# Kernel tuning notes

Hardware: AMD Instinct MI355X
Metric: run time of the kernel (lower is better)

Reference implementation:

```python
import jax, jax.numpy as jnp
import numpy as np

B, C, H, W = 2, 512, 64, 64
NUM_GROUPS = 32
EPS = 1e-6


def setup_inputs() -> dict:
    key = jax.random.key(0)
    ks = jax.random.split(key, 6)
    s = 1.0 / np.sqrt(C)
    return {
        "x": jax.random.normal(ks[0], (B, C, H, W), dtype=jnp.float32),
        "gn_scale": jnp.ones((C,), jnp.float32),
        "gn_bias": jnp.zeros((C,), jnp.float32),
        "wq": jax.random.normal(ks[1], (C, C), jnp.float32) * s,
        "bq": jnp.zeros((C,), jnp.float32),
        "wk": jax.random.normal(ks[2], (C, C), jnp.float32) * s,
        "bk": jnp.zeros((C,), jnp.float32),
        "wv": jax.random.normal(ks[3], (C, C), jnp.float32) * s,
        "bv": jnp.zeros((C,), jnp.float32),
        "wp": jax.random.normal(ks[4], (C, C), jnp.float32) * s,
        "bp": jnp.zeros((C,), jnp.float32),
    }


def group_norm(x, scale, bias):
    # x: [b, c, h, w]; GroupNorm with NUM_GROUPS groups, eps=1e-6, affine
    b, c, h, w = x.shape
    xg = x.reshape(b, NUM_GROUPS, c // NUM_GROUPS, h, w)
    mean = jnp.mean(xg, axis=(2, 3, 4), keepdims=True)
    var = jnp.var(xg, axis=(2, 3, 4), keepdims=True)
    xg = (xg - mean) * jax.lax.rsqrt(var + EPS)
    xn = xg.reshape(b, c, h, w)
    return xn * scale[None, :, None, None] + bias[None, :, None, None]


def reference(x, gn_scale, gn_bias, wq, bq, wk, bk, wv, bv, wp, bp):
    b, c, h, w = x.shape
    n = h * w
    hn = group_norm(x, gn_scale, gn_bias).reshape(b, c, n)  # [b,c,n]
    # 1x1 convs == per-pixel linear over channels
    q = jnp.einsum('dc,bcn->bdn', wq, hn) + bq[None, :, None]
    k = jnp.einsum('dc,bcn->bdn', wk, hn) + bk[None, :, None]
    v = jnp.einsum('dc,bcn->bdn', wv, hn) + bv[None, :, None]
    # attn[b,i,j] = softmax_j( q[:, :, i] . k[:, :, j] / sqrt(c) )
    attn = jnp.einsum('bci,bcj->bij', q, k) * (float(c) ** -0.5)
    attn = jax.nn.softmax(attn, axis=-1)
    out = jnp.einsum('bcj,bij->bci', v, attn)  # [b,c,n]
    out = jnp.einsum('dc,bcn->bdn', wp, out) + bp[None, :, None]
    return x + out.reshape(b, c, h, w)
```

## Files before the change

kernel.cpp:

```cpp
#include <hip/hip_runtime.h>

typedef __bf16 bf16x8 __attribute__((ext_vector_type(8)));
typedef float f32x4 __attribute__((ext_vector_type(4)));
typedef int i32x8 __attribute__((ext_vector_type(8)));


#if defined(__has_builtin)
#if __has_builtin(__builtin_amdgcn_global_load_lds)
#define HAS_GLL 1
#endif
#endif

__device__ __forceinline__ void async_copy16(const void* g, void* l) {
#ifdef HAS_GLL
    __builtin_amdgcn_global_load_lds(
        (const __attribute__((address_space(1))) unsigned int*)g,
        (__attribute__((address_space(3))) unsigned int*)l, 16, 0, 0);
#else
    *(int4*)l = *(const int4*)g;
#endif
}

__device__ __forceinline__ unsigned char to_fp8(float v) {
    return (unsigned char)(__builtin_amdgcn_cvt_pk_fp8_f32(v, v, 0, false) & 0xFF);
}

#define MXSCALE 0x7F7F7F7F

__global__ __launch_bounds__(256) void prep_kernel(
    const float* __restrict__ x, float* __restrict__ ps,
    const float* __restrict__ wq, const float* __restrict__ wk,
    const float* __restrict__ wv, const float* __restrict__ wp,
    const float* __restrict__ bq, const float* __restrict__ bk,
    unsigned char* __restrict__ wqk8, unsigned char* __restrict__ wv8,
    __bf16* __restrict__ wp_b, float* __restrict__ bqk) {
    if (blockIdx.x >= 1024) {
        int idx = (blockIdx.x - 1024) * 256 + threadIdx.x;
        wqk8[idx] = to_fp8(wq[idx]);
        wqk8[262144 + idx] = to_fp8(wk[idx]);
        wv8[idx] = to_fp8(wv[idx]);
        wp_b[idx] = (__bf16)wp[idx];
        if (idx < 512) {
            bqk[idx] = bq[idx];
            bqk[512 + idx] = bk[idx];
        }
        return;
    }
    int blk = blockIdx.x;
    const float4* base = (const float4*)x + (size_t)blk * 1024;
    float s1 = 0.f, s2 = 0.f;
#pragma unroll
    for (int i = 0; i < 4; ++i) {
        float4 v = base[threadIdx.x + (i << 8)];
        s1 += v.x + v.y + v.z + v.w;
        s2 += v.x * v.x + v.y * v.y + v.z * v.z + v.w * v.w;
    }
    for (int off = 32; off >= 1; off >>= 1) {
        s1 += __shfl_xor(s1, off);
        s2 += __shfl_xor(s2, off);
    }
    __shared__ float r1[4], r2[4];
    int wave = threadIdx.x >> 6, lane = threadIdx.x & 63;
    if (lane == 0) { r1[wave] = s1; r2[wave] = s2; }
    __syncthreads();
    if (threadIdx.x == 0) {
        ps[blk] = r1[0] + r1[1] + r1[2] + r1[3];
        ps[1024 + blk] = r2[0] + r2[1] + r2[2] + r2[3];
    }
}

__global__ __launch_bounds__(256) void gn_apply_kernel(const float* __restrict__ x,
                                                       const float* __restrict__ gn_scale,
                                                       const float* __restrict__ gn_bias,
                                                       const float* __restrict__ ps,
                                                       unsigned char* __restrict__ hn8) {
    __shared__ float tile[32][33];
    int b = blockIdx.z;
    int n0 = blockIdx.x * 32, c0 = blockIdx.y * 32;
    int tx = threadIdx.x & 31, ty = threadIdx.x >> 5;
    const float* xb = x + (size_t)b * 512 * 4096;
#pragma unroll
    for (int r = 0; r < 4; ++r) {
        int c = ty + r * 8;
        tile[c][tx] = xb[(size_t)(c0 + c) * 4096 + n0 + tx];
    }
    int c = c0 + tx;
    int g = (b << 5) + (c >> 4);
    float s1 = 0.f, s2 = 0.f;
#pragma unroll
    for (int i = 0; i < 16; ++i) {
        s1 += ps[(g << 4) + i];
        s2 += ps[1024 + (g << 4) + i];
    }
    float m = s1 * (1.f / 65536.f);
    float var = s2 * (1.f / 65536.f) - m * m;
    float rs = rsqrtf(var + 1e-6f);
    float sc = gn_scale[c] * rs;
    float bi = gn_bias[c] - m * sc;
    __syncthreads();
    unsigned char* outp = hn8 + (size_t)b * 4096 * 512;
#pragma unroll
    for (int r = 0; r < 4; ++r) {
        int n = ty + r * 8;
        float v = tile[tx][n];
        outp[(size_t)(n0 + n) * 512 + c] = to_fp8(v * sc + bi);
    }
}

template <int BN, int OUT_MODE, int BIAS_MODE>
__device__ __forceinline__ void mx_gemm_body(
    const unsigned char* __restrict__ Ab, int lda,
    const unsigned char* __restrict__ Bb, int ldb,
    void* __restrict__ C, int ldc,
    const float* __restrict__ bias, int K, float scale,
    long m0, long n0, unsigned char* As, unsigned char* Bs) {
    constexpr int NT = BN / 32;
    constexpr int BSZ = BN * 128;
    const int tid = threadIdx.x;
    const int lane = tid & 63, wave = tid >> 6;
    const int ln = lane & 15, q = lane >> 4;
    const int wm = (wave >> 1) << 6;
    const int wn = (wave & 1) * (BN / 2);

    f32x4 acc[4][NT] = {};

#pragma unroll
    for (int p = 0; p < 4; ++p) {
        int c = (p << 8) + tid;
        int row = c >> 3, sg = ((c & 7) ^ (row & 7)) << 4;
        async_copy16(Ab + (long)row * lda + sg, &As[c << 4]);
    }
#pragma unroll
    for (int p = 0; p < NT; ++p) {
        int c = (p << 8) + tid;
        int row = c >> 3, sg = ((c & 7) ^ (row & 7)) << 4;
        async_copy16(Bb + (long)row * ldb + sg, &Bs[c << 4]);
    }

    const int nk = K >> 7;
    for (int ki = 0; ki < nk; ++ki) {
        __syncthreads();
        const int cur = ki & 1;
        if (ki + 1 < nk) {
            const int k1 = (ki + 1) << 7;
            unsigned char* Ad = As + (cur ^ 1) * 16384;
            unsigned char* Bd = Bs + (cur ^ 1) * BSZ;
#pragma unroll
            for (int p = 0; p < 4; ++p) {
                int c = (p << 8) + tid;
                int row = c >> 3, sg = ((c & 7) ^ (row & 7)) << 4;
                async_copy16(Ab + (long)row * lda + k1 + sg, Ad + (c << 4));
            }
#pragma unroll
            for (int p = 0; p < NT; ++p) {
                int c = (p << 8) + tid;
                int row = c >> 3, sg = ((c & 7) ^ (row & 7)) << 4;
                async_copy16(Bb + (long)row * ldb + k1 + sg, Bd + (c << 4));
            }
        }
        const unsigned char* Ar = As + cur * 16384;
        const unsigned char* Br = Bs + cur * BSZ;
        i32x8 af[4], bf[NT];
#pragma unroll
        for (int t = 0; t < 4; ++t) {
            int row = wm + t * 16 + ln, e = row & 7;
            const unsigned char* ap = Ar + (row << 7);
            *(int4*)&af[t] = *(const int4*)(ap + ((((q << 1)) ^ e) << 4));
            *((int4*)&af[t] + 1) = *(const int4*)(ap + ((((q << 1) | 1) ^ e) << 4));
        }
#pragma unroll
        for (int t = 0; t < NT; ++t) {
            int row = wn + t * 16 + ln, e = row & 7;
            const unsigned char* bp = Br + (row << 7);
            *(int4*)&bf[t] = *(const int4*)(bp + ((((q << 1)) ^ e) << 4));
            *((int4*)&bf[t] + 1) = *(const int4*)(bp + ((((q << 1) | 1) ^ e) << 4));
        }
#pragma unroll
        for (int mt = 0; mt < 4; ++mt)
#pragma unroll
            for (int nt = 0; nt < NT; ++nt)
                acc[mt][nt] = __builtin_amdgcn_mfma_scale_f32_16x16x128_f8f6f4(
                    af[mt], bf[nt], acc[mt][nt], 0, 0, 0, MXSCALE, 0, MXSCALE);
    }

#pragma unroll
    for (int mt = 0; mt < 4; ++mt) {
#pragma unroll
        for (int nt = 0; nt < NT; ++nt) {
            long col = n0 + wn + nt * 16 + ln;
#pragma unroll
            for (int r = 0; r < 4; ++r) {
                long row = m0 + wm + mt * 16 + (q << 2) + r;
                float v = acc[mt][nt][r] * scale;
                if (BIAS_MODE == 1) v += bias[row];
                if (BIAS_MODE == 2) v += bias[col];
                long off = row * (long)ldc + col;
                if (OUT_MODE == 0) {
                    ((unsigned char*)C)[off] = to_fp8(v);
                } else {
                    ((_Float16*)C)[off] = (_Float16)v;
                }
            }
        }
    }
}

__global__ __launch_bounds__(256) void qkv_kernel(
    const unsigned char* __restrict__ hn8, const unsigned char* __restrict__ wqk8,
    const unsigned char* __restrict__ wv8, const float* __restrict__ bqk,
    const float* __restrict__ bv, unsigned char* __restrict__ qk8,
    unsigned char* __restrict__ v8) {
    __shared__ __align__(16) unsigned char As[2 * 128 * 128];
    __shared__ __align__(16) unsigned char Bs[2 * 128 * 128];
    int z = blockIdx.z;
    if (z < 2) {
        long b = z;
        long m0 = (long)blockIdx.y * 128, n0 = (long)blockIdx.x * 128;
        mx_gemm_body<128, 0, 2>(hn8 + b * 4096 * 512 + m0 * 512, 512,
                                wqk8 + n0 * 512, 512,
                                qk8 + b * 4096 * 1024, 1024,
                                bqk, 512, 1.f, m0, n0, As, Bs);
    } else {
        long b = z - 2;
        int flat = blockIdx.y * 8 + blockIdx.x;
        long m0 = (long)(flat >> 6) * 128, n0 = (long)(flat & 63) * 64;
        mx_gemm_body<64, 0, 1>(wv8 + m0 * 512, 512,
                               hn8 + b * 4096 * 512 + n0 * 512, 512,
                               v8 + b * 512 * 4096, 4096,
                               bv, 512, 1.f, m0, n0, As, Bs);
    }
}

__global__ __launch_bounds__(256) void mx_s_kernel(const unsigned char* __restrict__ QK,
                                                   unsigned char* __restrict__ S,
                                                   float scale) {
    __shared__ __align__(16) unsigned char As[2 * 128 * 128];
    __shared__ __align__(16) unsigned char Bs[2 * 128 * 128];
    long b = blockIdx.z;
    long m0 = (long)blockIdx.y * 128, n0 = (long)blockIdx.x * 128;
    mx_gemm_body<128, 0, 0>(QK + b * 4096 * 1024 + m0 * 1024, 1024,
                            QK + b * 4096 * 1024 + n0 * 1024 + 512, 1024,
                            S + b * 4096 * 4096, 4096,
                            nullptr, 512, scale, m0, n0, As, Bs);
}

#define CVT4(dst, base, word)                                   \
    dst[base + 0] = __builtin_amdgcn_cvt_f32_fp8(word, 0);      \
    dst[base + 1] = __builtin_amdgcn_cvt_f32_fp8(word, 1);      \
    dst[base + 2] = __builtin_amdgcn_cvt_f32_fp8(word, 2);      \
    dst[base + 3] = __builtin_amdgcn_cvt_f32_fp8(word, 3);

__global__ __launch_bounds__(256) void softmax_kernel(unsigned char* __restrict__ S) {
    long row = blockIdx.x;
    unsigned char* srow = S + (row << 12);
    int tid = threadIdx.x;
    int4 d = ((const int4*)srow)[tid];
    float v[16];
    CVT4(v, 0, d.x)
    CVT4(v, 4, d.y)
    CVT4(v, 8, d.z)
    CVT4(v, 12, d.w)
    float mx = -1e30f;
#pragma unroll
    for (int p = 0; p < 16; ++p) mx = fmaxf(mx, v[p]);
    for (int off = 32; off >= 1; off >>= 1) mx = fmaxf(mx, __shfl_xor(mx, off));
    __shared__ float red[4], red2[4];
    int wave = tid >> 6, lane = tid & 63;
    if (lane == 0) red[wave] = mx;
    __syncthreads();
    mx = fmaxf(fmaxf(red[0], red[1]), fmaxf(red[2], red[3]));
    float s = 0.f;
#pragma unroll
    for (int p = 0; p < 16; ++p) {
        v[p] = __expf(v[p] - mx);
        s += v[p];
    }
    for (int off = 32; off >= 1; off >>= 1) s += __shfl_xor(s, off);
    if (lane == 0) red2[wave] = s;
    __syncthreads();
    s = red2[0] + red2[1] + red2[2] + red2[3];
    float inv64 = 64.f / s;
    int w[4];
#pragma unroll
    for (int i = 0; i < 4; ++i) {
        w[i] = __builtin_amdgcn_cvt_pk_fp8_f32(v[4 * i] * inv64, v[4 * i + 1] * inv64, 0, false);
        w[i] = __builtin_amdgcn_cvt_pk_fp8_f32(v[4 * i + 2] * inv64, v[4 * i + 3] * inv64, w[i], true);
    }
    ((int4*)srow)[tid] = make_int4(w[0], w[1], w[2], w[3]);
}

__global__ __launch_bounds__(256) void mx_pv_kernel(const unsigned char* __restrict__ P,
                                                    const unsigned char* __restrict__ V,
                                                    __bf16* __restrict__ O) {
    __shared__ __align__(16) unsigned char As[2 * 128 * 128];
    __shared__ __align__(16) unsigned char Bs[2 * 64 * 128];
    const int tid = threadIdx.x;
    const int lane = tid & 63, wave = tid >> 6;
    const int ln = lane & 15, q = lane >> 4;
    const int wm = (wave >> 1) << 6, wn = (wave & 1) << 5;
    const int b = blockIdx.x >> 5;
    const long m0 = (long)(blockIdx.x & 31) * 128;
    const long n0 = (long)blockIdx.y * 64;
    const unsigned char* Pb = P + ((long)b * 4096 + m0) * 4096;
    const unsigned char* Vb = V + ((long)b * 512 + n0) * 4096;

    f32x4 acc[4][2] = {};

#pragma unroll
    for (int p = 0; p < 4; ++p) {
        int c = (p << 8) + tid;
        int row = c >> 3, sg = ((c & 7) ^ (row & 7)) << 4;
        async_copy16(Pb + (long)row * 4096 + sg, &As[c << 4]);
    }
#pragma unroll
    for (int p = 0; p < 2; ++p) {
        int c = (p << 8) + tid;
        int row = c >> 3, sg = ((c & 7) ^ (row & 7)) << 4;
        async_copy16(Vb + (long)row * 4096 + sg, &Bs[c << 4]);
    }

    for (int ki = 0; ki < 32; ++ki) {
        __syncthreads();
        const int cur = ki & 1;
        if (ki + 1 < 32) {
            const int k1 = (ki + 1) << 7;
            unsigned char* Ad = As + (cur ^ 1) * 16384;
            unsigned char* Bd = Bs + (cur ^ 1) * 8192;
#pragma unroll
            for (int p = 0; p < 4; ++p) {
                int c = (p << 8) + tid;
                int row = c >> 3, sg = ((c & 7) ^ (row & 7)) << 4;
                async_copy16(Pb + (long)row * 4096 + k1 + sg, Ad + (c << 4));
            }
#pragma unroll
            for (int p = 0; p < 2; ++p) {
                int c = (p << 8) + tid;
                int row = c >> 3, sg = ((c & 7) ^ (row & 7)) << 4;
                async_copy16(Vb + (long)row * 4096 + k1 + sg, Bd + (c << 4));
            }
        }
        const unsigned char* Ar = As + cur * 16384;
        const unsigned char* Br = Bs + cur * 8192;
        i32x8 af[4], bf[2];
#pragma unroll
        for (int t = 0; t < 4; ++t) {
            int row = wm + t * 16 + ln, e = row & 7;
            const unsigned char* ap = Ar + (row << 7);
            *(int4*)&af[t] = *(const int4*)(ap + ((((q << 1)) ^ e) << 4));
            *((int4*)&af[t] + 1) = *(const int4*)(ap + ((((q << 1) | 1) ^ e) << 4));
        }
#pragma unroll
        for (int t = 0; t < 2; ++t) {
            int row = wn + t * 16 + ln, e = row & 7;
            const unsigned char* bp = Br + (row << 7);
            *(int4*)&bf[t] = *(const int4*)(bp + ((((q << 1)) ^ e) << 4));
            *((int4*)&bf[t] + 1) = *(const int4*)(bp + ((((q << 1) | 1) ^ e) << 4));
        }
#pragma unroll
        for (int mt = 0; mt < 4; ++mt)
#pragma unroll
            for (int nt = 0; nt < 2; ++nt)
                acc[mt][nt] = __builtin_amdgcn_mfma_scale_f32_16x16x128_f8f6f4(
                    af[mt], bf[nt], acc[mt][nt], 0, 0, 0, MXSCALE, 0, MXSCALE);
    }

    __bf16* Ob = O + (long)b * 4096 * 512;
#pragma unroll
    for (int mt = 0; mt < 4; ++mt) {
#pragma unroll
        for (int nt = 0; nt < 2; ++nt) {
            long col = n0 + wn + nt * 16 + ln;
#pragma unroll
            for (int r = 0; r < 4; ++r) {
                long row = m0 + wm + mt * 16 + (q << 2) + r;
                Ob[row * 512 + col] = (__bf16)(acc[mt][nt][r] * 0.015625f);
            }
        }
    }
}

__global__ __launch_bounds__(256) void proj_kernel(
    const __bf16* __restrict__ A, const __bf16* __restrict__ Bt, long bsB,
    float* __restrict__ C, long bsC, const float* __restrict__ bias,
    const float* __restrict__ resid) {
    __shared__ __align__(16) __bf16 As[128][64];
    __shared__ __align__(16) __bf16 Bs[64][64];
    const int tid = threadIdx.x;
    const int wave = tid >> 6, lane = tid & 63;
    const int q = lane >> 4, ln = lane & 15;
    const int wm = wave << 5;
    const long m0 = (long)blockIdx.y * 128, n0 = (long)blockIdx.x * 64;
    const int b = blockIdx.z;
    const __bf16* Ab = A + m0 * 512;
    const __bf16* Bb = Bt + (long)b * bsB + n0 * 512;

    f32x4 acc[2][4] = {};

    for (int k0 = 0; k0 < 512; k0 += 64) {
        __syncthreads();
#pragma unroll
        for (int p = 0; p < 4; ++p) {
            int c = (p << 8) + tid;
            int row = c >> 3, sg = (c & 7) << 3;
            async_copy16(Ab + (long)row * 512 + k0 + sg, &As[0][0] + (c << 3));
        }
#pragma unroll
        for (int p = 0; p < 2; ++p) {
            int c = (p << 8) + tid;
            int row = c >> 3, sg = (c & 7) << 3;
            async_copy16(Bb + (long)row * 512 + k0 + sg, &Bs[0][0] + (c << 3));
        }
        __syncthreads();
#pragma unroll
        for (int kk = 0; kk < 2; ++kk) {
            bf16x8 af[2], bfr[4];
#pragma unroll
            for (int mt = 0; mt < 2; ++mt)
                af[mt] = *(const bf16x8*)(&As[wm + mt * 16 + ln][(kk << 5) + (q << 3)]);
#pragma unroll
            for (int nt = 0; nt < 4; ++nt)
                bfr[nt] = *(const bf16x8*)(&Bs[nt * 16 + ln][(kk << 5) + (q << 3)]);
#pragma unroll
            for (int mt = 0; mt < 2; ++mt)
#pragma unroll
                for (int nt = 0; nt < 4; ++nt)
                    acc[mt][nt] = __builtin_amdgcn_mfma_f32_16x16x32_bf16(
                        af[mt], bfr[nt], acc[mt][nt], 0, 0, 0);
        }
    }

#pragma unroll
    for (int mt = 0; mt < 2; ++mt) {
#pragma unroll
        for (int nt = 0; nt < 4; ++nt) {
            long col = n0 + nt * 16 + ln;
#pragma unroll
            for (int r = 0; r < 4; ++r) {
                long row = m0 + wm + mt * 16 + (q << 2) + r;
                long off = (long)b * bsC + row * 4096 + col;
                C[off] = acc[mt][nt][r] + bias[row] + resid[off];
            }
        }
    }
}

extern "C" void kernel_launch(void* const* d_in, const int* in_sizes, int n_in,
                              void* d_out, int out_size, void* d_ws, size_t ws_size,
                              hipStream_t stream) {
    const float* x = (const float*)d_in[0];
    const float* gn_scale = (const float*)d_in[1];
    const float* gn_bias = (const float*)d_in[2];
    const float* wq = (const float*)d_in[3];
    const float* bq = (const float*)d_in[4];
    const float* wk = (const float*)d_in[5];
    const float* bk = (const float*)d_in[6];
    const float* wv = (const float*)d_in[7];
    const float* bv = (const float*)d_in[8];
    const float* wp = (const float*)d_in[9];
    const float* bp = (const float*)d_in[10];
    float* out = (float*)d_out;

    char* ws = (char*)d_ws;
    unsigned char* wqk8 = (unsigned char*)(ws + 0x0);
    unsigned char* wv8 = (unsigned char*)(ws + 0x80000);
    __bf16* wp_b = (__bf16*)(ws + 0xC0000);
    float* bqk = (float*)(ws + 0x140000);
    float* psum = (float*)(ws + 0x142000);
    unsigned char* hn8 = (unsigned char*)(ws + 0x150000);
    unsigned char* qk8 = (unsigned char*)(ws + 0x550000);
    unsigned char* v8 = (unsigned char*)(ws + 0xD50000);
    __bf16* o_t = (__bf16*)(ws + 0x1150000);
    unsigned char* S8 = (unsigned char*)(ws + 0x1950000);
    (void)ws_size;

    prep_kernel<<<2048, 256, 0, stream>>>(x, psum, wq, wk, wv, wp, bq, bk,
                                          wqk8, wv8, wp_b, bqk);
    gn_apply_kernel<<<dim3(128, 16, 2), 256, 0, stream>>>(x, gn_scale, gn_bias,
                                                          psum, hn8);

    qkv_kernel<<<dim3(8, 32, 4), 256, 0, stream>>>(hn8, wqk8, wv8, bqk, bv,
                                                   qk8, v8);

    const float attn_scale = 0.044194173824159216f;
    mx_s_kernel<<<dim3(32, 32, 2), 256, 0, stream>>>(qk8, S8, attn_scale);
    softmax_kernel<<<8192, 256, 0, stream>>>(S8);
    mx_pv_kernel<<<dim3(64, 8), 256, 0, stream>>>(S8, v8, o_t);

    proj_kernel<<<dim3(64, 4, 2), 256, 0, stream>>>(
        wp_b, o_t, 4096l * 512, out, 512l * 4096, bp, x);
}
```

Measured before the change: 191.8 us.

## Fuse softmax into QK^T GEMM with per-panel stats and MX-scaled PV rescale

Removes the standalone softmax pass by computing per-128-column-panel row maxima (rounded up to powers of two) and partial sums in the S GEMM epilogue, writing unnormalized fp8 probabilities. The PV kernel combines the panel statistics into per-row power-of-two block scales, applies them through the MX scale operand of the fp8 MFMA, and divides by the global denominator in its epilogue. This avoids a full read-modify-write of the 4096x4096 fp8 score matrix. It also deepens the GEMM pipeline with explicit vmcnt waits, a prefetch two stages ahead, and raised wave priority around the MFMAs. The trade-offs are added workspace, grid swizzling, and fp8 precision that now depends on the per-panel exponent choice.

```diff
diff --git a/kernel.cpp b/kernel.cpp
--- a/kernel.cpp
+++ b/kernel.cpp
@@ -26,6 +26,9 @@
 }
 
 #define MXSCALE 0x7F7F7F7F
+
+#define ASM_VMCNT(N) asm volatile("s_waitcnt vmcnt(" #N ")" ::: "memory")
+#define ASM_LGKM0() asm volatile("s_waitcnt lgkmcnt(0)" ::: "memory")
 
 __global__ __launch_bounds__(256) void prep_kernel(
     const float* __restrict__ x, float* __restrict__ ps,
@@ -124,40 +127,37 @@
 
     f32x4 acc[4][NT] = {};
 
-#pragma unroll
-    for (int p = 0; p < 4; ++p) {
-        int c = (p << 8) + tid;
-        int row = c >> 3, sg = ((c & 7) ^ (row & 7)) << 4;
-        async_copy16(Ab + (long)row * lda + sg, &As[c << 4]);
-    }
-#pragma unroll
-    for (int p = 0; p < NT; ++p) {
-        int c = (p << 8) + tid;
-        int row = c >> 3, sg = ((c & 7) ^ (row & 7)) << 4;
-        async_copy16(Bb + (long)row * ldb + sg, &Bs[c << 4]);
-    }
+    auto stage = [&](int kt, int buf) {
+        const int k0 = kt << 7;
+        unsigned char* Ad = As + buf * 16384;
+        unsigned char* Bd = Bs + buf * BSZ;
+#pragma unroll
+        for (int p = 0; p < 4; ++p) {
+            int c = (p << 8) + tid;
+            int row = c >> 3, sg = ((c & 7) ^ (row & 7)) << 4;
+            async_copy16(Ab + (long)row * lda + k0 + sg, Ad + (c << 4));
+        }
+#pragma unroll
+        for (int p = 0; p < NT; ++p) {
+            int c = (p << 8) + tid;
+            int row = c >> 3, sg = ((c & 7) ^ (row & 7)) << 4;
+            async_copy16(Bb + (long)row * ldb + k0 + sg, Bd + (c << 4));
+        }
+    };
 
     const int nk = K >> 7;
+    stage(0, 0);
+    if (nk > 1) stage(1, 1);
+
     for (int ki = 0; ki < nk; ++ki) {
-        __syncthreads();
+        if (ki < nk - 1) {
+            if constexpr (NT == 4) ASM_VMCNT(8);
+            else ASM_VMCNT(6);
+        } else {
+            ASM_VMCNT(0);
+        }
+        __builtin_amdgcn_s_barrier();
         const int cur = ki & 1;
-        if (ki + 1 < nk) {
-            const int k1 = (ki + 1) << 7;
-            unsigned char* Ad = As + (cur ^ 1) * 16384;
-            unsigned char* Bd = Bs + (cur ^ 1) * BSZ;
-#pragma unroll
-            for (int p = 0; p < 4; ++p) {
-                int c = (p << 8) + tid;
-                int row = c >> 3, sg = ((c & 7) ^ (row & 7)) << 4;
-                async_copy16(Ab + (long)row * lda + k1 + sg, Ad + (c << 4));
-            }
-#pragma unroll
-            for (int p = 0; p < NT; ++p) {
-                int c = (p << 8) + tid;
-                int row = c >> 3, sg = ((c & 7) ^ (row & 7)) << 4;
-                async_copy16(Bb + (long)row * ldb + k1 + sg, Bd + (c << 4));
-            }
-        }
         const unsigned char* Ar = As + cur * 16384;
         const unsigned char* Br = Bs + cur * BSZ;
         i32x8 af[4], bf[NT];
@@ -175,12 +175,17 @@
             *(int4*)&bf[t] = *(const int4*)(bp + ((((q << 1)) ^ e) << 4));
             *((int4*)&bf[t] + 1) = *(const int4*)(bp + ((((q << 1) | 1) ^ e) << 4));
         }
+        ASM_LGKM0();
+        __builtin_amdgcn_s_barrier();
+        if (ki + 2 < nk) stage(ki + 2, cur);
+        __builtin_amdgcn_s_setprio(1);
 #pragma unroll
         for (int mt = 0; mt < 4; ++mt)
 #pragma unroll
             for (int nt = 0; nt < NT; ++nt)
                 acc[mt][nt] = __builtin_amdgcn_mfma_scale_f32_16x16x128_f8f6f4(
                     af[mt], bf[nt], acc[mt][nt], 0, 0, 0, MXSCALE, 0, MXSCALE);
+        __builtin_amdgcn_s_setprio(0);
     }
 
 #pragma unroll
@@ -197,8 +202,10 @@
                 long off = row * (long)ldc + col;
                 if (OUT_MODE == 0) {
                     ((unsigned char*)C)[off] = to_fp8(v);
+                } else if (OUT_MODE == 1) {
+                    ((_Float16*)C)[off] = (_Float16)v;
                 } else {
-                    ((_Float16*)C)[off] = (_Float16)v;
+                    ((__bf16*)C)[off] = (__bf16)v;
                 }
             }
         }
@@ -231,69 +238,171 @@
     }
 }
 
-__global__ __launch_bounds__(256) void mx_s_kernel(const unsigned char* __restrict__ QK,
-                                                   unsigned char* __restrict__ S,
-                                                   float scale) {
+__global__ __launch_bounds__(256) void mx_s_softmax_kernel(
+    const unsigned char* __restrict__ QK, unsigned char* __restrict__ P8,
+    float* __restrict__ pmaxF, float* __restrict__ psumF, float scale) {
     __shared__ __align__(16) unsigned char As[2 * 128 * 128];
     __shared__ __align__(16) unsigned char Bs[2 * 128 * 128];
-    long b = blockIdx.z;
-    long m0 = (long)blockIdx.y * 128, n0 = (long)blockIdx.x * 128;
-    mx_gemm_body<128, 0, 0>(QK + b * 4096 * 1024 + m0 * 1024, 1024,
-                            QK + b * 4096 * 1024 + n0 * 1024 + 512, 1024,
-                            S + b * 4096 * 4096, 4096,
-                            nullptr, 512, scale, m0, n0, As, Bs);
-}
-
-#define CVT4(dst, base, word)                                   \
-    dst[base + 0] = __builtin_amdgcn_cvt_f32_fp8(word, 0);      \
-    dst[base + 1] = __builtin_amdgcn_cvt_f32_fp8(word, 1);      \
-    dst[base + 2] = __builtin_amdgcn_cvt_f32_fp8(word, 2);      \
-    dst[base + 3] = __builtin_amdgcn_cvt_f32_fp8(word, 3);
-
-__global__ __launch_bounds__(256) void softmax_kernel(unsigned char* __restrict__ S) {
-    long row = blockIdx.x;
-    unsigned char* srow = S + (row << 12);
-    int tid = threadIdx.x;
-    int4 d = ((const int4*)srow)[tid];
-    float v[16];
-    CVT4(v, 0, d.x)
-    CVT4(v, 4, d.y)
-    CVT4(v, 8, d.z)
-    CVT4(v, 12, d.w)
-    float mx = -1e30f;
-#pragma unroll
-    for (int p = 0; p < 16; ++p) mx = fmaxf(mx, v[p]);
-    for (int off = 32; off >= 1; off >>= 1) mx = fmaxf(mx, __shfl_xor(mx, off));
-    __shared__ float red[4], red2[4];
-    int wave = tid >> 6, lane = tid & 63;
-    if (lane == 0) red[wave] = mx;
+    __shared__ float sm_max[4][64], sm_sum[4][64];
+    int id = (blockIdx.x & 7) * 256 + (blockIdx.x >> 3);
+    int mg = id >> 5;
+    long b = mg >> 5;
+    long m0 = (long)(mg & 31) * 128;
+    int panel = id & 31;
+    long n0 = (long)panel * 128;
+    const unsigned char* Ab = QK + b * 4096 * 1024 + m0 * 1024;
+    const unsigned char* Bb = QK + b * 4096 * 1024 + n0 * 1024 + 512;
+
+    const int tid = threadIdx.x;
+    const int lane = tid & 63, wave = tid >> 6;
+    const int ln = lane & 15, q = lane >> 4;
+    const int wm = (wave >> 1) << 6;
+    const int wn = (wave & 1) * 64;
+
+    f32x4 acc[4][4] = {};
+
+    auto stage = [&](int kt, int buf) {
+        const int k0 = kt << 7;
+        unsigned char* Ad = As + buf * 16384;
+        unsigned char* Bd = Bs + buf * 16384;
+#pragma unroll
+        for (int p = 0; p < 4; ++p) {
+            int c = (p << 8) + tid;
+            int row = c >> 3, sg = ((c & 7) ^ (row & 7)) << 4;
+            async_copy16(Ab + (long)row * 1024 + k0 + sg, Ad + (c << 4));
+        }
+#pragma unroll
+        for (int p = 0; p < 4; ++p) {
+            int c = (p << 8) + tid;
+            int row = c >> 3, sg = ((c & 7) ^ (row & 7)) << 4;
+            async_copy16(Bb + (long)row * 1024 + k0 + sg, Bd + (c << 4));
+        }
+    };
+
+    stage(0, 0);
+    stage(1, 1);
+    for (int ki = 0; ki < 4; ++ki) {
+        if (ki < 3) ASM_VMCNT(8);
+        else ASM_VMCNT(0);
+        __builtin_amdgcn_s_barrier();
+        const int cur = ki & 1;
+        const unsigned char* Ar = As + cur * 16384;
+        const unsigned char* Br = Bs + cur * 16384;
+        i32x8 af[4], bf[4];
+#pragma unroll
+        for (int t = 0; t < 4; ++t) {
+            int row = wm + t * 16 + ln, e = row & 7;
+            const unsigned char* ap = Ar + (row << 7);
+            *(int4*)&af[t] = *(const int4*)(ap + ((((q << 1)) ^ e) << 4));
+            *((int4*)&af[t] + 1) = *(const int4*)(ap + ((((q << 1) | 1) ^ e) << 4));
+        }
+#pragma unroll
+        for (int t = 0; t < 4; ++t) {
+            int row = wn + t * 16 + ln, e = row & 7;
+            const unsigned char* bp = Br + (row << 7);
+            *(int4*)&bf[t] = *(const int4*)(bp + ((((q << 1)) ^ e) << 4));
+            *((int4*)&bf[t] + 1) = *(const int4*)(bp + ((((q << 1) | 1) ^ e) << 4));
+        }
+        ASM_LGKM0();
+        __builtin_amdgcn_s_barrier();
+        if (ki + 2 < 4) stage(ki + 2, cur);
+        __builtin_amdgcn_s_setprio(1);
+#pragma unroll
+        for (int mt = 0; mt < 4; ++mt)
+#pragma unroll
+            for (int nt = 0; nt < 4; ++nt)
+                acc[mt][nt] = __builtin_amdgcn_mfma_scale_f32_16x16x128_f8f6f4(
+                    af[mt], bf[nt], acc[mt][nt], 0, 0, 0, MXSCALE, 0, MXSCALE);
+        __builtin_amdgcn_s_setprio(0);
+    }
+
+    constexpr float L2E = 1.4426950408889634f;
+#pragma unroll
+    for (int mt = 0; mt < 4; ++mt)
+#pragma unroll
+        for (int nt = 0; nt < 4; ++nt)
+#pragma unroll
+            for (int r = 0; r < 4; ++r) acc[mt][nt][r] *= scale;
+    float mx4[4][4];
+#pragma unroll
+    for (int mt = 0; mt < 4; ++mt)
+#pragma unroll
+        for (int r = 0; r < 4; ++r) {
+            float m = acc[mt][0][r];
+#pragma unroll
+            for (int nt = 1; nt < 4; ++nt) m = fmaxf(m, acc[mt][nt][r]);
+#pragma unroll
+            for (int off = 1; off <= 8; off <<= 1) m = fmaxf(m, __shfl_xor(m, off));
+            mx4[mt][r] = m;
+        }
+    if (ln == 0) {
+#pragma unroll
+        for (int mt = 0; mt < 4; ++mt)
+#pragma unroll
+            for (int r = 0; r < 4; ++r) sm_max[wave][mt * 16 + (q << 2) + r] = mx4[mt][r];
+    }
     __syncthreads();
-    mx = fmaxf(fmaxf(red[0], red[1]), fmaxf(red[2], red[3]));
-    float s = 0.f;
-#pragma unroll
-    for (int p = 0; p < 16; ++p) {
-        v[p] = __expf(v[p] - mx);
-        s += v[p];
-    }
-    for (int off = 32; off >= 1; off >>= 1) s += __shfl_xor(s, off);
-    if (lane == 0) red2[wave] = s;
+    float mtl[4][4];
+#pragma unroll
+    for (int mt = 0; mt < 4; ++mt)
+#pragma unroll
+        for (int r = 0; r < 4; ++r) {
+            int i = mt * 16 + (q << 2) + r;
+            mtl[mt][r] = ceilf(fmaxf(sm_max[wave][i], sm_max[wave ^ 1][i]) * L2E);
+        }
+    unsigned char* Pw = P8 + b * 4096 * 4096;
+    float ps4[4][4] = {};
+#pragma unroll
+    for (int mt = 0; mt < 4; ++mt) {
+#pragma unroll
+        for (int nt = 0; nt < 4; ++nt) {
+            long col = n0 + wn + nt * 16 + ln;
+#pragma unroll
+            for (int r = 0; r < 4; ++r) {
+                long row = m0 + wm + mt * 16 + (q << 2) + r;
+                float p = exp2f(acc[mt][nt][r] * L2E - mtl[mt][r]);
+                ps4[mt][r] += p;
+                Pw[row * 4096 + col] = to_fp8(p);
+            }
+        }
+    }
+#pragma unroll
+    for (int mt = 0; mt < 4; ++mt)
+#pragma unroll
+        for (int r = 0; r < 4; ++r) {
+            float s = ps4[mt][r];
+#pragma unroll
+            for (int off = 1; off <= 8; off <<= 1) s += __shfl_xor(s, off);
+            ps4[mt][r] = s;
+        }
+    if (ln == 0) {
+#pragma unroll
+        for (int mt = 0; mt < 4; ++mt)
+#pragma unroll
+            for (int r = 0; r < 4; ++r) sm_sum[wave][mt * 16 + (q << 2) + r] = ps4[mt][r];
+    }
     __syncthreads();
-    s = red2[0] + red2[1] + red2[2] + red2[3];
-    float inv64 = 64.f / s;
-    int w[4];
-#pragma unroll
-    for (int i = 0; i < 4; ++i) {
-        w[i] = __builtin_amdgcn_cvt_pk_fp8_f32(v[4 * i] * inv64, v[4 * i + 1] * inv64, 0, false);
-        w[i] = __builtin_amdgcn_cvt_pk_fp8_f32(v[4 * i + 2] * inv64, v[4 * i + 3] * inv64, w[i], true);
-    }
-    ((int4*)srow)[tid] = make_int4(w[0], w[1], w[2], w[3]);
-}
-
-__global__ __launch_bounds__(256) void mx_pv_kernel(const unsigned char* __restrict__ P,
-                                                    const unsigned char* __restrict__ V,
-                                                    __bf16* __restrict__ O) {
+    if ((wave & 1) == 0 && ln == 0) {
+#pragma unroll
+        for (int mt = 0; mt < 4; ++mt)
+#pragma unroll
+            for (int r = 0; r < 4; ++r) {
+                int i = mt * 16 + (q << 2) + r;
+                long rowg = b * 4096 + m0 + wm + i;
+                pmaxF[rowg * 32 + panel] = mtl[mt][r];
+                psumF[rowg * 32 + panel] = sm_sum[wave][i] + sm_sum[wave ^ 1][i];
+            }
+    }
+}
+
+__global__ __launch_bounds__(256) void mx_pv_scaled_kernel(
+    const unsigned char* __restrict__ P, const unsigned char* __restrict__ V,
+    const float* __restrict__ pmaxF, const float* __restrict__ psumF,
+    __bf16* __restrict__ O) {
     __shared__ __align__(16) unsigned char As[2 * 128 * 128];
     __shared__ __align__(16) unsigned char Bs[2 * 64 * 128];
+    __shared__ __align__(16) unsigned char sb_lds[128 * 32];
+    __shared__ float inv_lds[128];
     const int tid = threadIdx.x;
     const int lane = tid & 63, wave = tid >> 6;
     const int ln = lane & 15, q = lane >> 4;
@@ -301,53 +410,76 @@
     const int b = blockIdx.x >> 5;
     const long m0 = (long)(blockIdx.x & 31) * 128;
     const long n0 = (long)blockIdx.y * 64;
-    const unsigned char* Pb = P + ((long)b * 4096 + m0) * 4096;
+    const long rowg0 = (long)b * 4096 + m0;
+
+    if (tid < 128) {
+        const float4* pm4 = (const float4*)(pmaxF + (rowg0 + tid) * 32);
+        const float4* ps4 = (const float4*)(psumF + (rowg0 + tid) * 32);
+        float4 pm[8], ps[8];
+#pragma unroll
+        for (int i = 0; i < 8; ++i) { pm[i] = pm4[i]; ps[i] = ps4[i]; }
+        float g = -1e30f;
+#pragma unroll
+        for (int i = 0; i < 8; ++i)
+            g = fmaxf(g, fmaxf(fmaxf(pm[i].x, pm[i].y), fmaxf(pm[i].z, pm[i].w)));
+        float denom = 0.f;
+        unsigned int* sbw = (unsigned int*)sb_lds + tid * 8;
+#pragma unroll
+        for (int i = 0; i < 8; ++i) {
+            float d0 = pm[i].x - g, d1 = pm[i].y - g, d2 = pm[i].z - g, d3 = pm[i].w - g;
+            denom += ps[i].x * exp2f(d0) + ps[i].y * exp2f(d1) +
+                     ps[i].z * exp2f(d2) + ps[i].w * exp2f(d3);
+            int b0 = 127 + (int)d0, b1 = 127 + (int)d1, b2 = 127 + (int)d2, b3 = 127 + (int)d3;
+            b0 = b0 < 0 ? 0 : b0; b1 = b1 < 0 ? 0 : b1;
+            b2 = b2 < 0 ? 0 : b2; b3 = b3 < 0 ? 0 : b3;
+            sbw[i] = (unsigned)b0 | ((unsigned)b1 << 8) | ((unsigned)b2 << 16) |
+                     ((unsigned)b3 << 24);
+        }
+        inv_lds[tid] = 1.f / denom;
+    }
+    __syncthreads();
+
+    const unsigned char* Pb = P + rowg0 * 4096;
     const unsigned char* Vb = V + ((long)b * 512 + n0) * 4096;
 
     f32x4 acc[4][2] = {};
 
-#pragma unroll
-    for (int p = 0; p < 4; ++p) {
-        int c = (p << 8) + tid;
-        int row = c >> 3, sg = ((c & 7) ^ (row & 7)) << 4;
-        async_copy16(Pb + (long)row * 4096 + sg, &As[c << 4]);
-    }
-#pragma unroll
-    for (int p = 0; p < 2; ++p) {
-        int c = (p << 8) + tid;
-        int row = c >> 3, sg = ((c & 7) ^ (row & 7)) << 4;
-        async_copy16(Vb + (long)row * 4096 + sg, &Bs[c << 4]);
-    }
-
+    auto stage = [&](int kt, int buf) {
+        const int k0 = kt << 7;
+        unsigned char* Ad = As + buf * 16384;
+        unsigned char* Bd = Bs + buf * 8192;
+#pragma unroll
+        for (int p = 0; p < 4; ++p) {
+            int c = (p << 8) + tid;
+            int row = c >> 3, sg = ((c & 7) ^ (row & 7)) << 4;
+            async_copy16(Pb + (long)row * 4096 + k0 + sg, Ad + (c << 4));
+        }
+#pragma unroll
+        for (int p = 0; p < 2; ++p) {
+            int c = (p << 8) + tid;
+            int row = c >> 3, sg = ((c & 7) ^ (row & 7)) << 4;
+            async_copy16(Vb + (long)row * 4096 + k0 + sg, Bd + (c << 4));
+        }
+    };
+
+    stage(0, 0);
+    stage(1, 1);
     for (int ki = 0; ki < 32; ++ki) {
-        __syncthreads();
+        if (ki < 31) ASM_VMCNT(6);
+        else ASM_VMCNT(0);
+        __builtin_amdgcn_s_barrier();
         const int cur = ki & 1;
-        if (ki + 1 < 32) {
-            const int k1 = (ki + 1) << 7;
-            unsigned char* Ad = As + (cur ^ 1) * 16384;
-            unsigned char* Bd = Bs + (cur ^ 1) * 8192;
-#pragma unroll
-            for (int p = 0; p < 4; ++p) {
-                int c = (p << 8) + tid;
-                int row = c >> 3, sg = ((c & 7) ^ (row & 7)) << 4;
-                async_copy16(Pb + (long)row * 4096 + k1 + sg, Ad + (c << 4));
-            }
-#pragma unroll
-            for (int p = 0; p < 2; ++p) {
-                int c = (p << 8) + tid;
-                int row = c >> 3, sg = ((c & 7) ^ (row & 7)) << 4;
-                async_copy16(Vb + (long)row * 4096 + k1 + sg, Bd + (c << 4));
-            }
-        }
         const unsigned char* Ar = As + cur * 16384;
         const unsigned char* Br = Bs + cur * 8192;
         i32x8 af[4], bf[2];
+        int saw[4];
 #pragma unroll
         for (int t = 0; t < 4; ++t) {
             int row = wm + t * 16 + ln, e = row & 7;
             const unsigned char* ap = Ar + (row << 7);
             *(int4*)&af[t] = *(const int4*)(ap + ((((q << 1)) ^ e) << 4));
             *((int4*)&af[t] + 1) = *(const int4*)(ap + ((((q << 1) | 1) ^ e) << 4));
+            saw[t] = (int)sb_lds[(row << 5) + ki] * 0x01010101;
         }
 #pragma unroll
         for (int t = 0; t < 2; ++t) {
@@ -356,12 +488,17 @@
             *(int4*)&bf[t] = *(const int4*)(bp + ((((q << 1)) ^ e) << 4));
             *((int4*)&bf[t] + 1) = *(const int4*)(bp + ((((q << 1) | 1) ^ e) << 4));
         }
+        ASM_LGKM0();
+        __builtin_amdgcn_s_barrier();
+        if (ki + 2 < 32) stage(ki + 2, cur);
+        __builtin_amdgcn_s_setprio(1);
 #pragma unroll
         for (int mt = 0; mt < 4; ++mt)
 #pragma unroll
             for (int nt = 0; nt < 2; ++nt)
                 acc[mt][nt] = __builtin_amdgcn_mfma_scale_f32_16x16x128_f8f6f4(
-                    af[mt], bf[nt], acc[mt][nt], 0, 0, 0, MXSCALE, 0, MXSCALE);
+                    af[mt], bf[nt], acc[mt][nt], 0, 0, 0, saw[mt], 0, MXSCALE);
+        __builtin_amdgcn_s_setprio(0);
     }
 
     __bf16* Ob = O + (long)b * 4096 * 512;
@@ -372,8 +509,8 @@
             long col = n0 + wn + nt * 16 + ln;
 #pragma unroll
             for (int r = 0; r < 4; ++r) {
-                long row = m0 + wm + mt * 16 + (q << 2) + r;
-                Ob[row * 512 + col] = (__bf16)(acc[mt][nt][r] * 0.015625f);
+                int rowl = wm + mt * 16 + (q << 2) + r;
+                Ob[(m0 + rowl) * 512 + col] = (__bf16)(acc[mt][nt][r] * inv_lds[rowl]);
             }
         }
     }
@@ -471,20 +608,22 @@
     unsigned char* v8 = (unsigned char*)(ws + 0xD50000);
     __bf16* o_t = (__bf16*)(ws + 0x1150000);
     unsigned char* S8 = (unsigned char*)(ws + 0x1950000);
+    float* pmaxF = (float*)(ws + 0x3950000);
+    float* psumF = (float*)(ws + 0x3A50000);
     (void)ws_size;
 
     prep_kernel<<<2048, 256, 0, stream>>>(x, psum, wq, wk, wv, wp, bq, bk,
                                           wqk8, wv8, wp_b, bqk);
     gn_apply_kernel<<<dim3(128, 16, 2), 256, 0, stream>>>(x, gn_scale, gn_bias,
                                                           psum, hn8);
-
     qkv_kernel<<<dim3(8, 32, 4), 256, 0, stream>>>(hn8, wqk8, wv8, bqk, bv,
                                                    qk8, v8);
 
     const float attn_scale = 0.044194173824159216f;
-    mx_s_kernel<<<dim3(32, 32, 2), 256, 0, stream>>>(qk8, S8, attn_scale);
-    softmax_kernel<<<8192, 256, 0, stream>>>(S8);
-    mx_pv_kernel<<<dim3(64, 8), 256, 0, stream>>>(S8, v8, o_t);
+    mx_s_softmax_kernel<<<2048, 256, 0, stream>>>(qk8, S8, pmaxF, psumF,
+                                                  attn_scale);
+    mx_pv_scaled_kernel<<<dim3(64, 8), 256, 0, stream>>>(S8, v8, pmaxF, psumF,
+                                                         o_t);
 
     proj_kernel<<<dim3(64, 4, 2), 256, 0, stream>>>(
         wp_b, o_t, 4096l * 512, out, 512l * 4096, bp, x);
```

New measurement: 192.7 us. Within noise of the previous version (+0.5%).
